# Optimization experiments

Measured on AMD Instinct MI355X. Metric: run time of the kernel, lower is better.

Reference implementation:

```python
import jax, jax.numpy as jnp
import numpy as np

B, L, D = 8, 8192, 512   # batch, seq_len (q_len == kv_len), model dim
H, K = 8, 64             # heads, head_dim
W = 128                  # chunk width == stride (non-overlapping chunks)


def setup_inputs() -> dict:
    key = jax.random.key(0)
    ks = jax.random.split(key, 6)
    s = 1.0 / np.sqrt(D)
    return {
        "inputs_q": jax.random.normal(ks[0], (B, L, D), jnp.float32),
        "inputs_kv": jax.random.normal(ks[1], (B, L, D), jnp.float32),
        "Wq": jax.random.normal(ks[2], (D, H, K), jnp.float32) * s,
        "Wk": jax.random.normal(ks[3], (D, H, K), jnp.float32) * s,
        "Wv": jax.random.normal(ks[4], (D, H, K), jnp.float32) * s,
        "Wo": jax.random.normal(ks[5], (H, K, D), jnp.float32) * s,
    }


def reference(inputs_q, inputs_kv, Wq, Wk, Wv, Wo):
    # LocalAttentionLayer with q/kv_chunk_width == stride == W and
    # always_attend_to_first_position=True. Since width == stride the chunks
    # are non-overlapping, so the per-chunk Python loop of the original is
    # equivalent to a batched reshape into [B, C, W, ...] chunks. QKV
    # projections are position-wise, so projecting the full sequence first is
    # exactly the same math as projecting each chunk.
    C = L // W  # number of chunks
    scale = 1.0 / jnp.sqrt(jnp.asarray(K, inputs_q.dtype))

    q = jnp.einsum('bld,dhk->blhk', inputs_q, Wq) * scale  # [B,L,H,K]
    k = jnp.einsum('bld,dhk->blhk', inputs_kv, Wk)
    v = jnp.einsum('bld,dhk->blhk', inputs_kv, Wv)

    qc = q.reshape(B, C, W, H, K)
    kc = k.reshape(B, C, W, H, K)
    vc = v.reshape(B, C, W, H, K)

    # Global first KV position ([CLS]) prepended to every chunk's keys/values,
    # matching `kv_cls = inputs_kv[..., 0:1, :]; concat([kv_cls, chunk])`.
    k_cls = jnp.broadcast_to(k[:, None, 0:1], (B, C, 1, H, K))
    v_cls = jnp.broadcast_to(v[:, None, 0:1], (B, C, 1, H, K))
    kc = jnp.concatenate([k_cls, kc], axis=2)  # [B,C,W+1,H,K]
    vc = jnp.concatenate([v_cls, vc], axis=2)

    scores = jnp.einsum('bcqhk,bcmhk->bchqm', qc, kc)  # [B,C,H,W,W+1]
    attn = jax.nn.softmax(scores, axis=-1)
    ctx = jnp.einsum('bchqm,bcmhk->bcqhk', attn, vc)   # [B,C,W,H,K]
    ctx = ctx.reshape(B, L, H, K)
    return jnp.einsum('blhk,hkd->bld', ctx, Wo)        # [B,L,D]
```

## Files before the change

kernel.cpp:

```cpp
#include <hip/hip_runtime.h>
#include <hip/hip_bf16.h>
#include <type_traits>

#define B_ 8
#define L_ 8192
#define D_ 512
#define H_ 8
#define KD_ 64
#define W_ 128
#define C_ 64
#define M_ (B_ * L_)
#define HK_ 512

typedef __bf16 bf16_t;
typedef __bf16 bf16x8 __attribute__((ext_vector_type(8)));
typedef float f32x4 __attribute__((ext_vector_type(4)));

#define GLOAD16(gp, lp)                                                        \
  __builtin_amdgcn_global_load_lds(                                            \
      (const __attribute__((address_space(1))) unsigned int*)(gp),             \
      (__attribute__((address_space(3))) unsigned int*)(lp), 16, 0, 0)

__global__ void prep_weights_kernel(const float* __restrict__ Wq,
                                    const float* __restrict__ Wk,
                                    const float* __restrict__ Wv,
                                    const float* __restrict__ Wo,
                                    bf16_t* __restrict__ wt) {
  const int n = blockIdx.x;
  const int mat = blockIdx.y;
  const float* src = (mat == 0) ? Wq : (mat == 1) ? Wk : (mat == 2) ? Wv : Wo;
  const float scale = (mat == 0) ? 0.125f : 1.0f;
  bf16_t* dst = wt + ((size_t)mat * 512 + n) * 512;
  for (int d = threadIdx.x; d < 512; d += blockDim.x) {
    dst[d] = (bf16_t)(src[(size_t)d * 512 + n] * scale);
  }
}

__global__ void cvt_x_kernel(const float* __restrict__ xq,
                             const float* __restrict__ xkv,
                             bf16_t* __restrict__ oq,
                             bf16_t* __restrict__ okv) {
  const float* src = blockIdx.y ? xkv : xq;
  bf16_t* dst = blockIdx.y ? okv : oq;
  const size_t e = ((size_t)blockIdx.x * blockDim.x + threadIdx.x) * 8;
  float4 a = *reinterpret_cast<const float4*>(src + e);
  float4 b = *reinterpret_cast<const float4*>(src + e + 4);
  bf16x8 o;
  o[0] = (bf16_t)a.x; o[1] = (bf16_t)a.y; o[2] = (bf16_t)a.z; o[3] = (bf16_t)a.w;
  o[4] = (bf16_t)b.x; o[5] = (bf16_t)b.y; o[6] = (bf16_t)b.z; o[7] = (bf16_t)b.w;
  *reinterpret_cast<bf16x8*>(dst + e) = o;
}

template <typename OT, int NX>
__global__ __launch_bounds__(256, 3)
void gemm_bt16(const bf16_t* __restrict__ A0, const bf16_t* __restrict__ A1,
               const bf16_t* __restrict__ BT,
               OT* __restrict__ C0, OT* __restrict__ C1, OT* __restrict__ C2) {
  __shared__ bf16_t sA[128 * 64];
  __shared__ bf16_t sB[128 * 64];

  const int nb = gridDim.x;
  const int chunk = nb >> 3;
  const int bid = blockIdx.x;
  const int swz = (bid & 7) * chunk + (bid >> 3);
  const int my = swz / NX;
  const int mx = swz - my * NX;
  const int m0 = my * 128;
  const int seg = mx >> 2;
  const int n0o = (mx & 3) * 128;
  const int nB0 = mx * 128;

  const bf16_t* const A = (seg == 0) ? A0 : A1;
  OT* const outp = (seg == 0) ? C0 : (seg == 1) ? C1 : C2;

  const int tid = threadIdx.x;
  const int lane = tid & 63;
  const int w = tid >> 6;
  const int wr = (w >> 1) * 64;
  const int wc = (w & 1) * 64;

  const int srow = tid >> 3;
  const int scol = (tid & 7) * 8;
  const int cl = lane & 15;
  const int g = lane >> 4;
  const int Kdim = 512;

  f32x4 acc[4][4] = {};

  for (int k0 = 0; k0 < Kdim; k0 += 64) {
#pragma unroll
    for (int i = 0; i < 4; i++) {
      const bf16_t* gp = A + (size_t)(m0 + i * 32 + srow) * Kdim + k0 + scol;
      char* lp = (char*)sA + i * 4096 + w * 1024;
      GLOAD16(gp, lp);
    }
#pragma unroll
    for (int i = 0; i < 4; i++) {
      const bf16_t* gp = BT + (size_t)(nB0 + i * 32 + srow) * Kdim + k0 + scol;
      char* lp = (char*)sB + i * 4096 + w * 1024;
      GLOAD16(gp, lp);
    }
    __syncthreads();

#pragma unroll
    for (int kk = 0; kk < 2; kk++) {
      bf16x8 afr[4], bfr[4];
#pragma unroll
      for (int t = 0; t < 4; t++)
        afr[t] = *reinterpret_cast<const bf16x8*>(
            &sA[(wr + t * 16 + cl) * 64 + kk * 32 + g * 8]);
#pragma unroll
      for (int t = 0; t < 4; t++)
        bfr[t] = *reinterpret_cast<const bf16x8*>(
            &sB[(wc + t * 16 + cl) * 64 + kk * 32 + g * 8]);
#pragma unroll
      for (int i = 0; i < 4; i++)
#pragma unroll
        for (int j = 0; j < 4; j++)
          acc[i][j] = __builtin_amdgcn_mfma_f32_16x16x32_bf16(afr[i], bfr[j],
                                                              acc[i][j], 0, 0, 0);
    }
    __syncthreads();
  }

  const int crow = (lane >> 4) * 4;
  const int ccol = lane & 15;
#pragma unroll
  for (int i = 0; i < 4; i++) {
#pragma unroll
    for (int j = 0; j < 4; j++) {
      const int gm = m0 + wr + i * 16 + crow;
      const int gn = n0o + wc + j * 16 + ccol;
#pragma unroll
      for (int jj = 0; jj < 4; jj++) {
        const float vv = acc[i][j][jj];
        if constexpr (std::is_same<OT, float>::value)
          outp[(size_t)(gm + jj) * 512 + gn] = vv;
        else
          outp[(size_t)(gm + jj) * 512 + gn] = (bf16_t)vv;
      }
    }
  }
}

__global__ __launch_bounds__(256, 3)
void attn_kernel(const bf16_t* __restrict__ q, const bf16_t* __restrict__ k,
                 const bf16_t* __restrict__ v, bf16_t* __restrict__ ctx) {
  const int bid = blockIdx.x;
  const int swz = (bid & 7) * 512 + (bid >> 3);
  const int h = swz & 7;
  const int cb = swz >> 3;
  const int c = cb & 63;
  const int b = cb >> 6;

  const int tid = threadIdx.x;
  const int lane = tid & 63;
  const int w = tid >> 6;
  const int cl = lane & 15;
  const int g = lane >> 4;

  __shared__ bf16_t vT[64][136];
  __shared__ bf16_t pL[128][136];
  __shared__ float scl[128];
  __shared__ bf16_t kcls[64];
  __shared__ bf16_t vcls[64];

  const size_t headoff = (size_t)h * KD_;
  const size_t rowbase = (size_t)b * L_ + (size_t)c * W_;

  if (tid < 64) {
    kcls[tid] = k[(size_t)b * L_ * HK_ + headoff + tid];
    vcls[tid] = v[(size_t)b * L_ * HK_ + headoff + tid];
  }
  {
    const int m = tid >> 1;
    const int kd0 = (tid & 1) * 32;
    const bf16_t* vp = v + (rowbase + m) * HK_ + headoff + kd0;
#pragma unroll
    for (int i = 0; i < 4; i++) {
      bf16x8 t8 = *reinterpret_cast<const bf16x8*>(vp + i * 8);
#pragma unroll
      for (int j = 0; j < 8; j++) vT[kd0 + i * 8 + j][m] = t8[j];
    }
  }

  bf16x8 qf[2][2];
#pragma unroll
  for (int rt = 0; rt < 2; rt++)
#pragma unroll
    for (int kk = 0; kk < 2; kk++) {
      const size_t row = rowbase + w * 32 + rt * 16 + cl;
      qf[rt][kk] = *reinterpret_cast<const bf16x8*>(&q[row * HK_ + headoff + kk * 32 + g * 8]);
    }

  f32x4 sacc[2][8] = {};
#pragma unroll
  for (int ct = 0; ct < 8; ct++) {
    bf16x8 kf[2];
#pragma unroll
    for (int kk = 0; kk < 2; kk++) {
      const size_t rowm = rowbase + ct * 16 + cl;
      kf[kk] = *reinterpret_cast<const bf16x8*>(&k[rowm * HK_ + headoff + kk * 32 + g * 8]);
    }
#pragma unroll
    for (int rt = 0; rt < 2; rt++)
#pragma unroll
      for (int kk = 0; kk < 2; kk++)
        sacc[rt][ct] = __builtin_amdgcn_mfma_f32_16x16x32_bf16(qf[rt][kk], kf[kk], sacc[rt][ct], 0, 0, 0);
  }

  __syncthreads();

#pragma unroll
  for (int rt = 0; rt < 2; rt++) {
    float part = 0.f;
#pragma unroll
    for (int kk = 0; kk < 2; kk++)
#pragma unroll
      for (int j = 0; j < 8; j++)
        part += (float)qf[rt][kk][j] * (float)kcls[kk * 32 + g * 8 + j];
    part += __shfl_xor(part, 16);
    part += __shfl_xor(part, 32);
    if (g == 0) scl[w * 32 + rt * 16 + cl] = part;
  }

  float invd[2][4];
#pragma unroll
  for (int rt = 0; rt < 2; rt++) {
#pragma unroll
    for (int jj = 0; jj < 4; jj++) {
      float mx = sacc[rt][0][jj];
#pragma unroll
      for (int ct = 1; ct < 8; ct++) mx = fmaxf(mx, sacc[rt][ct][jj]);
#pragma unroll
      for (int d = 1; d < 16; d <<= 1) mx = fmaxf(mx, __shfl_xor(mx, d));
      const float sc = scl[w * 32 + rt * 16 + g * 4 + jj];
      mx = fmaxf(mx, sc);
      float sum = 0.f;
#pragma unroll
      for (int ct = 0; ct < 8; ct++) {
        const float e = __expf(sacc[rt][ct][jj] - mx);
        sacc[rt][ct][jj] = e;
        sum += e;
      }
#pragma unroll
      for (int d = 1; d < 16; d <<= 1) sum += __shfl_xor(sum, d);
      const float pc = __expf(sc - mx);
      sum += pc;
      const float inv = 1.0f / sum;
      invd[rt][jj] = inv;
      if (cl == 0) scl[w * 32 + rt * 16 + g * 4 + jj] = pc * inv;
    }
  }

#pragma unroll
  for (int rt = 0; rt < 2; rt++)
#pragma unroll
    for (int jj = 0; jj < 4; jj++) {
      const int row = w * 32 + rt * 16 + g * 4 + jj;
#pragma unroll
      for (int ct = 0; ct < 8; ct++)
        pL[row][ct * 16 + cl] = (bf16_t)(sacc[rt][ct][jj] * invd[rt][jj]);
    }
  __syncthreads();

  f32x4 cacc[2][4] = {};
#pragma unroll
  for (int kk = 0; kk < 4; kk++) {
    bf16x8 vf[4];
#pragma unroll
    for (int c2 = 0; c2 < 4; c2++)
      vf[c2] = *reinterpret_cast<const bf16x8*>(&vT[c2 * 16 + cl][kk * 32 + g * 8]);
#pragma unroll
    for (int rt = 0; rt < 2; rt++) {
      const bf16x8 pf = *reinterpret_cast<const bf16x8*>(&pL[w * 32 + rt * 16 + cl][kk * 32 + g * 8]);
#pragma unroll
      for (int c2 = 0; c2 < 4; c2++)
        cacc[rt][c2] = __builtin_amdgcn_mfma_f32_16x16x32_bf16(pf, vf[c2], cacc[rt][c2], 0, 0, 0);
    }
  }

#pragma unroll
  for (int rt = 0; rt < 2; rt++)
#pragma unroll
    for (int c2 = 0; c2 < 4; c2++)
#pragma unroll
      for (int jj = 0; jj < 4; jj++) {
        const int row = w * 32 + rt * 16 + g * 4 + jj;
        const int kd = c2 * 16 + cl;
        const float val = cacc[rt][c2][jj] + scl[row] * (float)vcls[kd];
        ctx[(rowbase + row) * HK_ + headoff + kd] = (bf16_t)val;
      }
}

extern "C" void kernel_launch(void* const* d_in, const int* in_sizes, int n_in,
                              void* d_out, int out_size, void* d_ws, size_t ws_size,
                              hipStream_t stream) {
  const float* Xq = (const float*)d_in[0];
  const float* Xkv = (const float*)d_in[1];
  const float* Wq = (const float*)d_in[2];
  const float* Wk = (const float*)d_in[3];
  const float* Wv = (const float*)d_in[4];
  const float* Wo = (const float*)d_in[5];
  float* out = (float*)d_out;

  char* ws = (char*)d_ws;
  bf16_t* wT = (bf16_t*)ws;
  size_t off = (size_t)4 * 512 * 512 * sizeof(bf16_t);
  bf16_t* xqb  = (bf16_t*)(ws + off); off += (size_t)M_ * D_ * 2;
  bf16_t* xkvb = (bf16_t*)(ws + off); off += (size_t)M_ * D_ * 2;
  bf16_t* qb = (bf16_t*)(ws + off); off += (size_t)M_ * HK_ * 2;
  bf16_t* kb = (bf16_t*)(ws + off); off += (size_t)M_ * HK_ * 2;
  bf16_t* vb = (bf16_t*)(ws + off);
  bf16_t* ctxb = xqb;

  bf16_t* wTqkv = wT;
  bf16_t* wTo = wT + (size_t)3 * 512 * 512;

  prep_weights_kernel<<<dim3(512, 4), 128, 0, stream>>>(Wq, Wk, Wv, Wo, wT);
  cvt_x_kernel<<<dim3(M_ * D_ / 8 / 256, 2), 256, 0, stream>>>(Xq, Xkv, xqb, xkvb);

  gemm_bt16<bf16_t, 12><<<dim3(12 * (M_ / 128)), 256, 0, stream>>>(
      xqb, xkvb, wTqkv, qb, kb, vb);

  attn_kernel<<<dim3(H_ * C_ * B_), 256, 0, stream>>>(qb, kb, vb, ctxb);

  gemm_bt16<float, 4><<<dim3(4 * (M_ / 128)), 256, 0, stream>>>(
      ctxb, ctxb, wTo, out, out, out);
}
```

Before: 386.9 us.

## Double-buffer GEMM LDS tiles with prefetch and XOR-swizzled layout

Rewrites the bf16 projection GEMM mainloop to use two LDS buffers, prefetching the k-tile two steps ahead with async global-to-LDS loads under manual vmcnt waits and barriers. LDS columns are XOR-swizzled to reduce bank conflicts on fragment reads, and MFMA sections run at raised wave priority. Doubling LDS use lowers the occupancy target from 3 to 2 blocks per CU, trading latency hiding through extra waves for explicit overlap within each block.

Result: no change. 383.5 us (-0.9%).

```diff
diff --git a/kernel.cpp b/kernel.cpp
--- a/kernel.cpp
+++ b/kernel.cpp
@@ -52,17 +52,15 @@
 }
 
 template <typename OT, int NX>
-__global__ __launch_bounds__(256, 3)
+__global__ __launch_bounds__(256, 2)
 void gemm_bt16(const bf16_t* __restrict__ A0, const bf16_t* __restrict__ A1,
                const bf16_t* __restrict__ BT,
                OT* __restrict__ C0, OT* __restrict__ C1, OT* __restrict__ C2) {
-  __shared__ bf16_t sA[128 * 64];
-  __shared__ bf16_t sB[128 * 64];
-
-  const int nb = gridDim.x;
-  const int chunk = nb >> 3;
+  __shared__ bf16_t sA[2][128 * 64];
+  __shared__ bf16_t sB[2][128 * 64];
+
   const int bid = blockIdx.x;
-  const int swz = (bid & 7) * chunk + (bid >> 3);
+  const int swz = (bid & 7) * (NX * 64) + (bid >> 3);
   const int my = swz / NX;
   const int mx = swz - my * NX;
   const int m0 = my * 128;
@@ -78,49 +76,75 @@
   const int w = tid >> 6;
   const int wr = (w >> 1) * 64;
   const int wc = (w & 1) * 64;
-
-  const int srow = tid >> 3;
-  const int scol = (tid & 7) * 8;
   const int cl = lane & 15;
   const int g = lane >> 4;
-  const int Kdim = 512;
+  const int c7 = cl & 7;
+
+  const int srow = lane >> 3;
+  const int scol = ((lane & 7) ^ srow) * 8;
+  const bf16_t* const Ab = A + (size_t)(m0 + w * 8 + srow) * 512 + scol;
+  const bf16_t* const Bb = BT + (size_t)(nB0 + w * 8 + srow) * 512 + scol;
+
+  auto STAGE = [&](int t, int p) {
+    const bf16_t* a = Ab + t * 64;
+    const bf16_t* b = Bb + t * 64;
+    char* la = (char*)&sA[p][0] + w * 1024;
+    char* lb = (char*)&sB[p][0] + w * 1024;
+#pragma unroll
+    for (int i = 0; i < 4; i++) GLOAD16(a + (size_t)i * 32 * 512, la + i * 4096);
+#pragma unroll
+    for (int i = 0; i < 4; i++) GLOAD16(b + (size_t)i * 32 * 512, lb + i * 4096);
+  };
 
   f32x4 acc[4][4] = {};
 
-  for (int k0 = 0; k0 < Kdim; k0 += 64) {
-#pragma unroll
-    for (int i = 0; i < 4; i++) {
-      const bf16_t* gp = A + (size_t)(m0 + i * 32 + srow) * Kdim + k0 + scol;
-      char* lp = (char*)sA + i * 4096 + w * 1024;
-      GLOAD16(gp, lp);
-    }
-#pragma unroll
-    for (int i = 0; i < 4; i++) {
-      const bf16_t* gp = BT + (size_t)(nB0 + i * 32 + srow) * Kdim + k0 + scol;
-      char* lp = (char*)sB + i * 4096 + w * 1024;
-      GLOAD16(gp, lp);
-    }
-    __syncthreads();
-
+  auto BODY = [&](int t, int p, bool stage_next) __attribute__((always_inline)) {
+    bf16x8 afr[2][4], bfr[2][4];
 #pragma unroll
     for (int kk = 0; kk < 2; kk++) {
-      bf16x8 afr[4], bfr[4];
-#pragma unroll
-      for (int t = 0; t < 4; t++)
-        afr[t] = *reinterpret_cast<const bf16x8*>(
-            &sA[(wr + t * 16 + cl) * 64 + kk * 32 + g * 8]);
-#pragma unroll
-      for (int t = 0; t < 4; t++)
-        bfr[t] = *reinterpret_cast<const bf16x8*>(
-            &sB[(wc + t * 16 + cl) * 64 + kk * 32 + g * 8]);
+#pragma unroll
+      for (int tt = 0; tt < 4; tt++) {
+        afr[kk][tt] = *reinterpret_cast<const bf16x8*>(
+            &sA[p][(wr + tt * 16 + cl) * 64 + (((kk * 4 + g) ^ c7)) * 8]);
+        bfr[kk][tt] = *reinterpret_cast<const bf16x8*>(
+            &sB[p][(wc + tt * 16 + cl) * 64 + (((kk * 4 + g) ^ c7)) * 8]);
+      }
+    }
+    asm volatile("s_waitcnt lgkmcnt(0)" ::: "memory");
+    __builtin_amdgcn_s_barrier();
+    asm volatile("" ::: "memory");
+    if (stage_next) STAGE(t + 2, p);
+    __builtin_amdgcn_s_setprio(1);
+#pragma unroll
+    for (int kk = 0; kk < 2; kk++)
 #pragma unroll
       for (int i = 0; i < 4; i++)
 #pragma unroll
         for (int j = 0; j < 4; j++)
-          acc[i][j] = __builtin_amdgcn_mfma_f32_16x16x32_bf16(afr[i], bfr[j],
-                                                              acc[i][j], 0, 0, 0);
-    }
-    __syncthreads();
+          acc[i][j] = __builtin_amdgcn_mfma_f32_16x16x32_bf16(
+              afr[kk][i], bfr[kk][j], acc[i][j], 0, 0, 0);
+    __builtin_amdgcn_s_setprio(0);
+  };
+
+  STAGE(0, 0);
+  STAGE(1, 1);
+  for (int t = 0; t < 6; ++t) {
+    asm volatile("s_waitcnt vmcnt(8)" ::: "memory");
+    __builtin_amdgcn_s_barrier();
+    asm volatile("" ::: "memory");
+    BODY(t, t & 1, true);
+  }
+  {
+    asm volatile("s_waitcnt vmcnt(8)" ::: "memory");
+    __builtin_amdgcn_s_barrier();
+    asm volatile("" ::: "memory");
+    BODY(6, 0, false);
+  }
+  {
+    asm volatile("s_waitcnt vmcnt(0)" ::: "memory");
+    __builtin_amdgcn_s_barrier();
+    asm volatile("" ::: "memory");
+    BODY(7, 1, false);
   }
 
   const int crow = (lane >> 4) * 4;
```

## Replace 128x128 GEMM with 256x256 double-buffered, pipelined MFMA kernel

Applied to the files above, without the earlier changes.

Swaps the projection GEMM for a 512-thread kernel computing 256x256 output tiles, with a double-buffered LDS ring filled by direct global-to-LDS loads. It uses an XOR-swizzled shared layout and interleaves fragment reads, next-stage loads and MFMA groups with explicit barriers, waitcnt and setprio. The goal is to hide global load latency, cut LDS bank conflicts and raise arithmetic intensity per tile. In exchange it uses more registers and LDS per block (128 KB), which lowers occupancy, and it depends on hand-tuned wait counts being correct.

Measured after the change: 366.8 us. -5.2%, faster.

```diff
diff --git a/kernel.cpp b/kernel.cpp
--- a/kernel.cpp
+++ b/kernel.cpp
@@ -20,6 +20,12 @@
   __builtin_amdgcn_global_load_lds(                                            \
       (const __attribute__((address_space(1))) unsigned int*)(gp),             \
       (__attribute__((address_space(3))) unsigned int*)(lp), 16, 0, 0)
+
+#define WAIT_LGKM0()                                                           \
+  do {                                                                         \
+    asm volatile("s_waitcnt lgkmcnt(0)" ::: "memory");                         \
+    __builtin_amdgcn_sched_barrier(0);                                         \
+  } while (0)
 
 __global__ void prep_weights_kernel(const float* __restrict__ Wq,
                                     const float* __restrict__ Wk,
@@ -51,86 +57,155 @@
   *reinterpret_cast<bf16x8*>(dst + e) = o;
 }
 
-template <typename OT, int NX>
-__global__ __launch_bounds__(256, 3)
-void gemm_bt16(const bf16_t* __restrict__ A0, const bf16_t* __restrict__ A1,
-               const bf16_t* __restrict__ BT,
-               OT* __restrict__ C0, OT* __restrict__ C1, OT* __restrict__ C2) {
-  __shared__ bf16_t sA[128 * 64];
-  __shared__ bf16_t sB[128 * 64];
-
-  const int nb = gridDim.x;
-  const int chunk = nb >> 3;
+__device__ __forceinline__ bf16x8 rdfrag(const bf16_t* region, int rowbase,
+                                         int lane) {
+  const int fr = lane & 15;
+  const int fs = (lane >> 4) ^ (lane & 3);
+  return *reinterpret_cast<const bf16x8*>(region + (rowbase + fr) * 32 + fs * 8);
+}
+
+template <typename OT, int NTILE>
+__global__ __launch_bounds__(512, 2)
+void gemm256(const bf16_t* __restrict__ A0, const bf16_t* __restrict__ A1,
+             const bf16_t* __restrict__ BT,
+             OT* __restrict__ C0, OT* __restrict__ C1, OT* __restrict__ C2) {
+  __shared__ bf16_t lds[8 * 8192];
+
+  constexpr int NB = NTILE * 256;
   const int bid = blockIdx.x;
-  const int swz = (bid & 7) * chunk + (bid >> 3);
-  const int my = swz / NX;
-  const int mx = swz - my * NX;
-  const int m0 = my * 128;
-  const int seg = mx >> 2;
-  const int n0o = (mx & 3) * 128;
-  const int nB0 = mx * 128;
+  const int swz = (bid & 7) * (NB / 8) + (bid >> 3);
+  const int my = swz / NTILE;
+  const int mx = swz - my * NTILE;
+  const int m0 = my * 256;
+  const int seg = mx >> 1;
+  const int ncol0 = (mx & 1) * 256;
+  const int nB0 = mx * 256;
 
   const bf16_t* const A = (seg == 0) ? A0 : A1;
   OT* const outp = (seg == 0) ? C0 : (seg == 1) ? C1 : C2;
 
   const int tid = threadIdx.x;
   const int lane = tid & 63;
-  const int w = tid >> 6;
-  const int wr = (w >> 1) * 64;
-  const int wc = (w & 1) * 64;
-
-  const int srow = tid >> 3;
-  const int scol = (tid & 7) * 8;
-  const int cl = lane & 15;
-  const int g = lane >> 4;
-  const int Kdim = 512;
-
-  f32x4 acc[4][4] = {};
-
-  for (int k0 = 0; k0 < Kdim; k0 += 64) {
-#pragma unroll
-    for (int i = 0; i < 4; i++) {
-      const bf16_t* gp = A + (size_t)(m0 + i * 32 + srow) * Kdim + k0 + scol;
-      char* lp = (char*)sA + i * 4096 + w * 1024;
-      GLOAD16(gp, lp);
-    }
-#pragma unroll
-    for (int i = 0; i < 4; i++) {
-      const bf16_t* gp = BT + (size_t)(nB0 + i * 32 + srow) * Kdim + k0 + scol;
-      char* lp = (char*)sB + i * 4096 + w * 1024;
-      GLOAD16(gp, lp);
-    }
-    __syncthreads();
-
-#pragma unroll
-    for (int kk = 0; kk < 2; kk++) {
-      bf16x8 afr[4], bfr[4];
-#pragma unroll
-      for (int t = 0; t < 4; t++)
-        afr[t] = *reinterpret_cast<const bf16x8*>(
-            &sA[(wr + t * 16 + cl) * 64 + kk * 32 + g * 8]);
-#pragma unroll
-      for (int t = 0; t < 4; t++)
-        bfr[t] = *reinterpret_cast<const bf16x8*>(
-            &sB[(wc + t * 16 + cl) * 64 + kk * 32 + g * 8]);
+  const int wid = tid >> 6;
+  const int wmB = (wid >> 2) * 128;
+  const int wnB = (wid & 3) * 64;
+
+  const int sr0 = tid >> 2;
+  const int sgs = (tid & 3) ^ (sr0 & 3);
+  const bf16_t* const Agb = A + ((size_t)m0 + sr0) * 512 + sgs * 8;
+  const bf16_t* const Bgb = BT + ((size_t)nB0 + sr0) * 512 + sgs * 8;
+
+  auto stage = [&](int tile, int mat, int kh) {
+    if (tile >= 8) return;
+    bf16_t* reg = lds + (((tile & 1) * 4) + mat * 2 + kh) * 8192;
+    const bf16_t* g0 = (mat == 0 ? Agb : Bgb) + tile * 64 + kh * 32;
+    char* lp = (char*)reg + wid * 1024;
+    GLOAD16(g0, lp);
+    GLOAD16(g0 + (size_t)128 * 512, lp + 8192);
+  };
+
+  f32x4 acc[8][4] = {};
+  bf16x8 a0[4], a1[4], a2[4], a3[4], b0[4], b2[4];
+
+  stage(0, 0, 0); stage(0, 1, 0); stage(0, 0, 1); stage(0, 1, 1);
+  stage(1, 1, 0); stage(1, 0, 0); stage(1, 1, 1);
+  asm volatile("s_waitcnt vmcnt(6)" ::: "memory");
+  __builtin_amdgcn_s_barrier();
+
+  for (int t = 0; t < 8; ++t) {
+    const int p = t & 1;
+    const bf16_t* Ap0 = lds + (p * 4 + 0) * 8192;
+    const bf16_t* Ap1 = lds + (p * 4 + 1) * 8192;
+    const bf16_t* Bp0 = lds + (p * 4 + 2) * 8192;
+    const bf16_t* Bp1 = lds + (p * 4 + 3) * 8192;
+
+#pragma unroll
+    for (int q = 0; q < 4; q++) a0[q] = rdfrag(Ap0, wmB + q * 16, lane);
+#pragma unroll
+    for (int q = 0; q < 4; q++) b0[q] = rdfrag(Bp0, wnB + q * 16, lane);
+    stage(t + 1, 0, 1);
+    __builtin_amdgcn_s_barrier();
+    WAIT_LGKM0();
+    if (t > 0) {
+      __builtin_amdgcn_s_setprio(1);
 #pragma unroll
       for (int i = 0; i < 4; i++)
 #pragma unroll
         for (int j = 0; j < 4; j++)
-          acc[i][j] = __builtin_amdgcn_mfma_f32_16x16x32_bf16(afr[i], bfr[j],
-                                                              acc[i][j], 0, 0, 0);
-    }
-    __syncthreads();
-  }
+          acc[i + 4][j] = __builtin_amdgcn_mfma_f32_16x16x32_bf16(
+              a3[i], b2[j], acc[i + 4][j], 0, 0, 0);
+      __builtin_amdgcn_s_setprio(0);
+    }
+    __builtin_amdgcn_s_barrier();
+
+#pragma unroll
+    for (int q = 0; q < 4; q++) a1[q] = rdfrag(Ap0, wmB + 64 + q * 16, lane);
+    stage(t + 2, 1, 0);
+    __builtin_amdgcn_s_barrier();
+    WAIT_LGKM0();
+    __builtin_amdgcn_s_setprio(1);
+#pragma unroll
+    for (int i = 0; i < 4; i++)
+#pragma unroll
+      for (int j = 0; j < 4; j++)
+        acc[i][j] = __builtin_amdgcn_mfma_f32_16x16x32_bf16(a0[i], b0[j],
+                                                            acc[i][j], 0, 0, 0);
+    __builtin_amdgcn_s_setprio(0);
+    __builtin_amdgcn_s_barrier();
+
+#pragma unroll
+    for (int q = 0; q < 4; q++) a2[q] = rdfrag(Ap1, wmB + q * 16, lane);
+#pragma unroll
+    for (int q = 0; q < 4; q++) b2[q] = rdfrag(Bp1, wnB + q * 16, lane);
+    stage(t + 2, 0, 0);
+    __builtin_amdgcn_s_barrier();
+    WAIT_LGKM0();
+    __builtin_amdgcn_s_setprio(1);
+#pragma unroll
+    for (int i = 0; i < 4; i++)
+#pragma unroll
+      for (int j = 0; j < 4; j++)
+        acc[i + 4][j] = __builtin_amdgcn_mfma_f32_16x16x32_bf16(
+            a1[i], b0[j], acc[i + 4][j], 0, 0, 0);
+    __builtin_amdgcn_s_setprio(0);
+    __builtin_amdgcn_s_barrier();
+
+#pragma unroll
+    for (int q = 0; q < 4; q++) a3[q] = rdfrag(Ap1, wmB + 64 + q * 16, lane);
+    stage(t + 2, 1, 1);
+    __builtin_amdgcn_s_barrier();
+    WAIT_LGKM0();
+    __builtin_amdgcn_s_setprio(1);
+#pragma unroll
+    for (int i = 0; i < 4; i++)
+#pragma unroll
+      for (int j = 0; j < 4; j++)
+        acc[i][j] = __builtin_amdgcn_mfma_f32_16x16x32_bf16(a2[i], b2[j],
+                                                            acc[i][j], 0, 0, 0);
+    __builtin_amdgcn_s_setprio(0);
+    if (t < 6) {
+      asm volatile("s_waitcnt vmcnt(6)" ::: "memory");
+    } else {
+      asm volatile("s_waitcnt vmcnt(0)" ::: "memory");
+    }
+    __builtin_amdgcn_s_barrier();
+  }
+
+#pragma unroll
+  for (int i = 0; i < 4; i++)
+#pragma unroll
+    for (int j = 0; j < 4; j++)
+      acc[i + 4][j] = __builtin_amdgcn_mfma_f32_16x16x32_bf16(
+          a3[i], b2[j], acc[i + 4][j], 0, 0, 0);
 
   const int crow = (lane >> 4) * 4;
   const int ccol = lane & 15;
 #pragma unroll
-  for (int i = 0; i < 4; i++) {
+  for (int i = 0; i < 8; i++) {
 #pragma unroll
     for (int j = 0; j < 4; j++) {
-      const int gm = m0 + wr + i * 16 + crow;
-      const int gn = n0o + wc + j * 16 + ccol;
+      const int gm = m0 + wmB + i * 16 + crow;
+      const int gn = ncol0 + wnB + j * 16 + ccol;
 #pragma unroll
       for (int jj = 0; jj < 4; jj++) {
         const float vv = acc[i][j][jj];
@@ -320,11 +395,11 @@
   prep_weights_kernel<<<dim3(512, 4), 128, 0, stream>>>(Wq, Wk, Wv, Wo, wT);
   cvt_x_kernel<<<dim3(M_ * D_ / 8 / 256, 2), 256, 0, stream>>>(Xq, Xkv, xqb, xkvb);
 
-  gemm_bt16<bf16_t, 12><<<dim3(12 * (M_ / 128)), 256, 0, stream>>>(
+  gemm256<bf16_t, 6><<<dim3(6 * (M_ / 256)), 512, 0, stream>>>(
       xqb, xkvb, wTqkv, qb, kb, vb);
 
   attn_kernel<<<dim3(H_ * C_ * B_), 256, 0, stream>>>(qb, kb, vb, ctxb);
 
-  gemm_bt16<float, 4><<<dim3(4 * (M_ / 128)), 256, 0, stream>>>(
+  gemm256<float, 2><<<dim3(2 * (M_ / 256)), 512, 0, stream>>>(
       ctxb, ctxb, wTo, out, out, out);
 }
```
